# Optimization experiments

Measured on AMD Instinct MI355X. Metric: run time of the kernel, lower is better.

The kernel has to match this reference:

```python
import jax, jax.numpy as jnp
import numpy as np


def gcn_conv(x, edge_index, W, b):
    """PyG-style GCNConv: add self-loops, symmetric deg normalization,
    linear transform, scatter-add aggregation at destination nodes."""
    N = x.shape[0]
    loops = jnp.arange(N)
    src = jnp.concatenate([edge_index[0], loops])  # [E+N]
    dst = jnp.concatenate([edge_index[1], loops])  # [E+N]
    deg = jax.ops.segment_sum(jnp.ones_like(dst, dtype=x.dtype), dst, num_segments=N)
    dinv = jnp.where(deg > 0, deg ** -0.5, jnp.zeros_like(deg))
    norm = dinv[src] * dinv[dst]  # [E+N]
    h = x @ W  # [N, H] transform before propagate (as in PyG GCNConv)
    out = jax.ops.segment_sum(h[src] * norm[:, None], dst, num_segments=N)
    return out + b


def setup_inputs() -> dict:
    key = jax.random.key(0)
    ks = jax.random.split(key, 9)
    N, E, F_in, H, F_out = 100000, 3200000, 128, 16, 128
    x = jax.random.normal(ks[0], (N, F_in), dtype=jnp.float32)
    edge_index = jax.random.randint(ks[1], (2, E), 0, N, dtype=jnp.int64)
    s = lambda k, shp, fan_in: jax.random.normal(k, shp, dtype=jnp.float32) / np.sqrt(fan_in)
    return {
        "x": x,
        "edge_index": edge_index,
        "W1": s(ks[2], (F_in, H), F_in),
        "b1": jnp.zeros((H,), jnp.float32),
        "W2": s(ks[3], (H, H), H),
        "b2": jnp.zeros((H,), jnp.float32),
        "W_lin": s(ks[4], (H, F_out), H),
        "b_lin": jnp.zeros((F_out,), jnp.float32),
    }


def reference(x, edge_index, W1, b1, W2, b2, W_lin, b_lin):
    h = jax.nn.relu(gcn_conv(x, edge_index, W1, b1))
    h = jax.nn.relu(gcn_conv(h, edge_index, W2, b2))
    return h @ W_lin + b_lin
```

## Files before the change

kernel.cpp:

```cpp
#include <hip/hip_runtime.h>
#include <hip/hip_fp16.h>


typedef int   v4i __attribute__((ext_vector_type(4)));
typedef float v4f __attribute__((ext_vector_type(4)));
typedef float v2f __attribute__((ext_vector_type(2)));

#define NPB        256
#define NPB_SHIFT  8
#define NB_MAX     512
#define BCAP       10240
#define PART_TILE  8192
#define PART_THR   1024
#define PT_ITERS   (PART_TILE / 4 / PART_THR)
#define FXSCALE    262144.0f
#define FXINV      (1.0f / 262144.0f)

__global__ __launch_bounds__(NB_MAX) void k_initcur(int* __restrict__ cur) {
    cur[threadIdx.x] = threadIdx.x * BCAP;
}

__global__ __launch_bounds__(PART_THR) void k_partition(const int* __restrict__ ei,
                                                        int* __restrict__ cur,
                                                        int* __restrict__ pairs, int E) {
    __shared__ int h[NB_MAX];
    __shared__ int rb[NB_MAX];
    int t = threadIdx.x;
    const v4i* s4 = (const v4i*)ei;
    const v4i* d4 = (const v4i*)(ei + E);
    int EQ = E >> 2;
    int q0 = blockIdx.x * (PART_TILE / 4);
    bool last = (blockIdx.x == gridDim.x - 1);
    v4i dsave[PT_ITERS];

    for (int j = t; j < NB_MAX; j += PART_THR) h[j] = 0;
    __syncthreads();
#pragma unroll
    for (int it = 0; it < PT_ITERS; ++it) {
        int q = q0 + it * PART_THR + t;
        v4i dd;
        if (q < EQ) {
            dd = __builtin_nontemporal_load(d4 + q);
            atomicAdd(&h[dd.x >> NPB_SHIFT], 1);
            atomicAdd(&h[dd.y >> NPB_SHIFT], 1);
            atomicAdd(&h[dd.z >> NPB_SHIFT], 1);
            atomicAdd(&h[dd.w >> NPB_SHIFT], 1);
        }
        dsave[it] = dd;
    }
    if (last) {
        for (int e = (EQ << 2) + t; e < E; e += PART_THR)
            atomicAdd(&h[ei[E + e] >> NPB_SHIFT], 1);
    }
    __syncthreads();
    for (int j = t; j < NB_MAX; j += PART_THR) {
        int c = h[j];
        rb[j] = c ? atomicAdd(&cur[j], c) : 0;
        h[j] = 0;
    }
    __syncthreads();
#pragma unroll
    for (int it = 0; it < PT_ITERS; ++it) {
        int q = q0 + it * PART_THR + t;
        if (q < EQ) {
            v4i ss = __builtin_nontemporal_load(s4 + q);
            v4i dd = dsave[it];
#pragma unroll
            for (int k = 0; k < 4; ++k) {
                int s = ss[k], d = dd[k];
                int b = d >> NPB_SHIFT;
                int pos = rb[b] + atomicAdd(&h[b], 1);
                pairs[pos] = (s << NPB_SHIFT) | (d & (NPB - 1));
            }
        }
    }
    if (last) {
        for (int e = (EQ << 2) + t; e < E; e += PART_THR) {
            int s = ei[e], d = ei[E + e];
            int b = d >> NPB_SHIFT;
            int pos = rb[b] + atomicAdd(&h[b], 1);
            pairs[pos] = (s << NPB_SHIFT) | (d & (NPB - 1));
        }
    }
}

__global__ __launch_bounds__(256) void k_deg(const int* __restrict__ pairs,
                                             const int* __restrict__ cur,
                                             float* __restrict__ dinv, int N) {
    __shared__ int deg[NPB];
    int b = blockIdx.x, t = threadIdx.x;
    int base = b * BCAP;
    int cnt  = cur[b] - base;
    deg[t] = 0;
    __syncthreads();
    const v4i* p4 = (const v4i*)(pairs + base);
    int cq = cnt >> 2;
    for (int q = t; q < cq; q += 256) {
        v4i pp = __builtin_nontemporal_load(p4 + q);
        atomicAdd(&deg[pp.x & (NPB - 1)], 1);
        atomicAdd(&deg[pp.y & (NPB - 1)], 1);
        atomicAdd(&deg[pp.z & (NPB - 1)], 1);
        atomicAdd(&deg[pp.w & (NPB - 1)], 1);
    }
    for (int i = (cq << 2) + t; i < cnt; i += 256)
        atomicAdd(&deg[pairs[base + i] & (NPB - 1)], 1);
    __syncthreads();
    int n = (b << NPB_SHIFT) + t;
    if (n < N) dinv[n] = rsqrtf((float)(deg[t] + 1));
}

__global__ __launch_bounds__(256) void k_xform1(const float* __restrict__ x,
                                                const float* __restrict__ W1,
                                                const float* __restrict__ dinv,
                                                __half* __restrict__ g, int N) {
    __shared__ float xs[16][132];
    __shared__ float ws[128 * 16];
    int t = threadIdx.x;
    int n0 = blockIdx.x * 16;
    const v4f* w4 = (const v4f*)W1;
    const v4f* x4 = (const v4f*)x;
    for (int idx = t; idx < 512; idx += 256) ((v4f*)ws)[idx] = w4[idx];
    for (int idx = t; idx < 512; idx += 256) {
        int r = idx >> 5, c4 = idx & 31;
        int n = n0 + r;
        v4f v = (n < N) ? x4[(size_t)n * 32 + c4] : (v4f)(0.f);
        *(v4f*)&xs[r][c4 * 4] = v;
    }
    __syncthreads();
    int node = t >> 4, f = t & 15;
    int n = n0 + node;
    if (n < N) {
        float sum = 0.f;
#pragma unroll
        for (int k = 0; k < 128; ++k) sum += xs[node][k] * ws[k * 16 + f];
        g[(size_t)n * 16 + f] = __float2half_rn(sum * dinv[n]);
    }
}

__device__ __forceinline__ v4i gather16(const __half* __restrict__ g, int p, int fo) {
    return *(const v4i*)(g + (size_t)(p >> NPB_SHIFT) * 16 + fo);
}
__device__ __forceinline__ void commit8(int* __restrict__ acc, int p, int fo, v4i r) {
    int* a = &acc[(p & (NPB - 1)) * 17 + fo];
#pragma unroll
    for (int j = 0; j < 4; ++j) {
        float2 f = __half22float2(((const __half2*)&r)[j]);
        atomicAdd(a + 2 * j,     __float2int_rn(f.x * FXSCALE));
        atomicAdd(a + 2 * j + 1, __float2int_rn(f.y * FXSCALE));
    }
}

__global__ __launch_bounds__(1024) void k_aggr1e(const __half* __restrict__ g1,
                                                 const int* __restrict__ pairs,
                                                 const int* __restrict__ cur,
                                                 const float* __restrict__ dinv,
                                                 const float* __restrict__ b1,
                                                 const float* __restrict__ W2,
                                                 __half* __restrict__ g2, int N) {
    __shared__ int   acc[NPB * 17];
    __shared__ float w2s[256];
    __shared__ float b1s[16];
    int t = threadIdx.x, b = blockIdx.x;
    int n0 = b << NPB_SHIFT;
    int base = b * BCAP;
    int cnt  = cur[b] - base;
    const int* pb = pairs + base;
    if (t < 256) w2s[t] = W2[t];
    if (t < 16)  b1s[t] = b1[t];
    for (int i = t; i < NPB * 17; i += 1024) acc[i] = 0;
    __syncthreads();
    int es = t >> 1, fo = (t & 1) << 3;
    int e = es;
    for (; e + 1536 < cnt; e += 2048) {
        int p0 = __builtin_nontemporal_load(pb + e);
        int p1 = __builtin_nontemporal_load(pb + e + 512);
        int p2 = __builtin_nontemporal_load(pb + e + 1024);
        int p3 = __builtin_nontemporal_load(pb + e + 1536);
        v4i r0 = gather16(g1, p0, fo);
        v4i r1 = gather16(g1, p1, fo);
        v4i r2 = gather16(g1, p2, fo);
        v4i r3 = gather16(g1, p3, fo);
        commit8(acc, p0, fo, r0);
        commit8(acc, p1, fo, r1);
        commit8(acc, p2, fo, r2);
        commit8(acc, p3, fo, r3);
    }
    for (; e < cnt; e += 512) {
        int p0 = pb[e];
        commit8(acc, p0, fo, gather16(g1, p0, fo));
    }
    __syncthreads();
#pragma unroll
    for (int r = 0; r < 4; ++r) {
        int idx = r * 1024 + t;
        int d = idx >> 4, f = idx & 15;
        int n = n0 + d;
        float hv = 0.f;
        if (n < N) {
            float sum  = (float)acc[d * 17 + f] * FXINV;
            float self = __half2float(g1[(size_t)n * 16 + f]);
            hv = fmaxf(dinv[n] * (sum + self) + b1s[f], 0.f);
        }
        acc[d * 17 + f] = __float_as_int(hv);
    }
    __syncthreads();
#pragma unroll
    for (int r = 0; r < 2; ++r) {
        int idx2 = r * 1024 + t;
        int d = idx2 >> 3, ff = idx2 & 7;
        int n = n0 + d;
        if (n < N) {
            float sx = 0.f, sy = 0.f;
#pragma unroll
            for (int k = 0; k < 16; ++k) {
                float hv = __int_as_float(acc[d * 17 + k]);
                sx += hv * w2s[k * 16 + 2 * ff];
                sy += hv * w2s[k * 16 + 2 * ff + 1];
            }
            float di = dinv[n];
            *(__half2*)(g2 + (size_t)n * 16 + 2 * ff) = __floats2half2_rn(sx * di, sy * di);
        }
    }
}

__global__ __launch_bounds__(1024) void k_aggr2e(const __half* __restrict__ g2,
                                                 const int* __restrict__ pairs,
                                                 const int* __restrict__ cur,
                                                 const float* __restrict__ dinv,
                                                 const float* __restrict__ b2,
                                                 const float* __restrict__ Wl,
                                                 const float* __restrict__ bl,
                                                 float* __restrict__ out, int N) {
    __shared__ int   acc[NPB * 17];
    __shared__ float wls[16 * 128];
    __shared__ float bls[128];
    __shared__ float b2s[16];
    int t = threadIdx.x, b = blockIdx.x;
    int n0 = b << NPB_SHIFT;
    int base = b * BCAP;
    int cnt  = cur[b] - base;
    const int* pb = pairs + base;
    if (t < 512) ((v4f*)wls)[t] = ((const v4f*)Wl)[t];
    if (t < 128) bls[t] = bl[t];
    if (t < 16)  b2s[t] = b2[t];
    for (int i = t; i < NPB * 17; i += 1024) acc[i] = 0;
    __syncthreads();
    int es = t >> 1, fo = (t & 1) << 3;
    int e = es;
    for (; e + 1536 < cnt; e += 2048) {
        int p0 = __builtin_nontemporal_load(pb + e);
        int p1 = __builtin_nontemporal_load(pb + e + 512);
        int p2 = __builtin_nontemporal_load(pb + e + 1024);
        int p3 = __builtin_nontemporal_load(pb + e + 1536);
        v4i r0 = gather16(g2, p0, fo);
        v4i r1 = gather16(g2, p1, fo);
        v4i r2 = gather16(g2, p2, fo);
        v4i r3 = gather16(g2, p3, fo);
        commit8(acc, p0, fo, r0);
        commit8(acc, p1, fo, r1);
        commit8(acc, p2, fo, r2);
        commit8(acc, p3, fo, r3);
    }
    for (; e < cnt; e += 512) {
        int p0 = pb[e];
        commit8(acc, p0, fo, gather16(g2, p0, fo));
    }
    __syncthreads();
#pragma unroll
    for (int r = 0; r < 4; ++r) {
        int idx = r * 1024 + t;
        int d = idx >> 4, f = idx & 15;
        int n = n0 + d;
        float hv = 0.f;
        if (n < N) {
            float sum  = (float)acc[d * 17 + f] * FXINV;
            float self = __half2float(g2[(size_t)n * 16 + f]);
            hv = fmaxf(dinv[n] * (sum + self) + b2s[f], 0.f);
        }
        acc[d * 17 + f] = __float_as_int(hv);
    }
    __syncthreads();
    const v2f* wl2 = (const v2f*)wls;
#pragma unroll
    for (int r = 0; r < 16; ++r) {
        int idx2 = r * 1024 + t;
        int d = idx2 >> 6, fc = idx2 & 63;
        int n = n0 + d;
        if (n < N) {
            float ox = bls[2 * fc], oy = bls[2 * fc + 1];
#pragma unroll
            for (int k = 0; k < 16; ++k) {
                float hv = __int_as_float(acc[d * 17 + k]);
                v2f w = wl2[k * 64 + fc];
                ox += hv * w.x;
                oy += hv * w.y;
            }
            v2f o; o.x = ox; o.y = oy;
            __builtin_nontemporal_store(o, (v2f*)(out + (size_t)n * 128 + 2 * fc));
        }
    }
}

extern "C" void kernel_launch(void* const* d_in, const int* in_sizes, int n_in,
                              void* d_out, int out_size, void* d_ws, size_t ws_size,
                              hipStream_t stream) {
    const float* x  = (const float*)d_in[0];
    const int*   ei = (const int*)d_in[1];
    const float* W1 = (const float*)d_in[2];
    const float* b1 = (const float*)d_in[3];
    const float* W2 = (const float*)d_in[4];
    const float* b2 = (const float*)d_in[5];
    const float* Wl = (const float*)d_in[6];
    const float* bl = (const float*)d_in[7];
    float*       out = (float*)d_out;

    const int N = in_sizes[0] / 128;
    const int E = in_sizes[1] / 2;
    const int NB = (N + NPB - 1) >> NPB_SHIFT;

    char* ws = (char*)d_ws;
    auto carve = [&](size_t bytes) {
        char* p = ws;
        ws += (bytes + 255) & ~(size_t)255;
        return p;
    };
    int*    cur   = (int*)carve((size_t)NB_MAX * 4);
    float*  dinv  = (float*)carve((size_t)N * 4);
    int*    pairs = (int*)carve((size_t)NB_MAX * BCAP * 4);
    __half* g1    = (__half*)carve((size_t)N * 16 * 2);
    __half* g2    = (__half*)carve((size_t)N * 16 * 2);
    (void)ws_size; (void)n_in; (void)out_size;

    k_initcur<<<1, NB_MAX, 0, stream>>>(cur);
    k_partition<<<(E + PART_TILE - 1) / PART_TILE, PART_THR, 0, stream>>>(ei, cur, pairs, E);
    k_deg<<<NB, 256, 0, stream>>>(pairs, cur, dinv, N);
    k_xform1<<<(N + 15) / 16, 256, 0, stream>>>(x, W1, dinv, g1, N);
    k_aggr1e<<<NB, 1024, 0, stream>>>(g1, pairs, cur, dinv, b1, W2, g2, N);
    k_aggr2e<<<NB, 1024, 0, stream>>>(g2, pairs, cur, dinv, b2, Wl, bl, out, N);
}
```

Before: 253.5 us.

## Halve destination bucket size and fold degree counting into partition kernel

Shrinks each destination bucket from 256 to 128 nodes, which doubles the bucket count (about 782 blocks instead of 391) and halves the aggregation block size to 512 threads, so more of the GPU is busy during the gather and scatter phases. It also drops the separate k_deg pass. In-degrees are now counted with global atomics inside k_partition, and dinv is computed in k_xform1. The cost is 3.2M global atomics on random addresses plus a memset, in place of one extra read of the pairs array. The smaller bucket capacity leaves less slack against overflow.

```diff
diff --git a/kernel.cpp b/kernel.cpp
--- a/kernel.cpp
+++ b/kernel.cpp
@@ -6,10 +6,10 @@
 typedef float v4f __attribute__((ext_vector_type(4)));
 typedef float v2f __attribute__((ext_vector_type(2)));
 
-#define NPB        256
-#define NPB_SHIFT  8
-#define NB_MAX     512
-#define BCAP       10240
+#define NPB        128
+#define NPB_SHIFT  7
+#define NB_MAX     1024
+#define BCAP       5632
 #define PART_TILE  8192
 #define PART_THR   1024
 #define PT_ITERS   (PART_TILE / 4 / PART_THR)
@@ -22,7 +22,8 @@
 
 __global__ __launch_bounds__(PART_THR) void k_partition(const int* __restrict__ ei,
                                                         int* __restrict__ cur,
-                                                        int* __restrict__ pairs, int E) {
+                                                        int* __restrict__ pairs,
+                                                        int* __restrict__ deg, int E) {
     __shared__ int h[NB_MAX];
     __shared__ int rb[NB_MAX];
     int t = threadIdx.x;
@@ -45,12 +46,19 @@
             atomicAdd(&h[dd.y >> NPB_SHIFT], 1);
             atomicAdd(&h[dd.z >> NPB_SHIFT], 1);
             atomicAdd(&h[dd.w >> NPB_SHIFT], 1);
+            atomicAdd(&deg[dd.x], 1);
+            atomicAdd(&deg[dd.y], 1);
+            atomicAdd(&deg[dd.z], 1);
+            atomicAdd(&deg[dd.w], 1);
         }
         dsave[it] = dd;
     }
     if (last) {
-        for (int e = (EQ << 2) + t; e < E; e += PART_THR)
-            atomicAdd(&h[ei[E + e] >> NPB_SHIFT], 1);
+        for (int e = (EQ << 2) + t; e < E; e += PART_THR) {
+            int d = ei[E + e];
+            atomicAdd(&h[d >> NPB_SHIFT], 1);
+            atomicAdd(&deg[d], 1);
+        }
     }
     __syncthreads();
     for (int j = t; j < NB_MAX; j += PART_THR) {
@@ -84,37 +92,14 @@
     }
 }
 
-__global__ __launch_bounds__(256) void k_deg(const int* __restrict__ pairs,
-                                             const int* __restrict__ cur,
-                                             float* __restrict__ dinv, int N) {
-    __shared__ int deg[NPB];
-    int b = blockIdx.x, t = threadIdx.x;
-    int base = b * BCAP;
-    int cnt  = cur[b] - base;
-    deg[t] = 0;
-    __syncthreads();
-    const v4i* p4 = (const v4i*)(pairs + base);
-    int cq = cnt >> 2;
-    for (int q = t; q < cq; q += 256) {
-        v4i pp = __builtin_nontemporal_load(p4 + q);
-        atomicAdd(&deg[pp.x & (NPB - 1)], 1);
-        atomicAdd(&deg[pp.y & (NPB - 1)], 1);
-        atomicAdd(&deg[pp.z & (NPB - 1)], 1);
-        atomicAdd(&deg[pp.w & (NPB - 1)], 1);
-    }
-    for (int i = (cq << 2) + t; i < cnt; i += 256)
-        atomicAdd(&deg[pairs[base + i] & (NPB - 1)], 1);
-    __syncthreads();
-    int n = (b << NPB_SHIFT) + t;
-    if (n < N) dinv[n] = rsqrtf((float)(deg[t] + 1));
-}
-
 __global__ __launch_bounds__(256) void k_xform1(const float* __restrict__ x,
                                                 const float* __restrict__ W1,
-                                                const float* __restrict__ dinv,
+                                                const int* __restrict__ deg,
+                                                float* __restrict__ dinv,
                                                 __half* __restrict__ g, int N) {
     __shared__ float xs[16][132];
     __shared__ float ws[128 * 16];
+    __shared__ float dvs[16];
     int t = threadIdx.x;
     int n0 = blockIdx.x * 16;
     const v4f* w4 = (const v4f*)W1;
@@ -126,6 +111,14 @@
         v4f v = (n < N) ? x4[(size_t)n * 32 + c4] : (v4f)(0.f);
         *(v4f*)&xs[r][c4 * 4] = v;
     }
+    if (t < 16) {
+        int n = n0 + t;
+        if (n < N) {
+            float dv = rsqrtf((float)(deg[n] + 1));
+            dinv[n] = dv;
+            dvs[t] = dv;
+        }
+    }
     __syncthreads();
     int node = t >> 4, f = t & 15;
     int n = n0 + node;
@@ -133,7 +126,7 @@
         float sum = 0.f;
 #pragma unroll
         for (int k = 0; k < 128; ++k) sum += xs[node][k] * ws[k * 16 + f];
-        g[(size_t)n * 16 + f] = __float2half_rn(sum * dinv[n]);
+        g[(size_t)n * 16 + f] = __float2half_rn(sum * dvs[node]);
     }
 }
 
@@ -150,13 +143,13 @@
     }
 }
 
-__global__ __launch_bounds__(1024) void k_aggr1e(const __half* __restrict__ g1,
-                                                 const int* __restrict__ pairs,
-                                                 const int* __restrict__ cur,
-                                                 const float* __restrict__ dinv,
-                                                 const float* __restrict__ b1,
-                                                 const float* __restrict__ W2,
-                                                 __half* __restrict__ g2, int N) {
+__global__ __launch_bounds__(512) void k_aggr1e(const __half* __restrict__ g1,
+                                                const int* __restrict__ pairs,
+                                                const int* __restrict__ cur,
+                                                const float* __restrict__ dinv,
+                                                const float* __restrict__ b1,
+                                                const float* __restrict__ W2,
+                                                __half* __restrict__ g2, int N) {
     __shared__ int   acc[NPB * 17];
     __shared__ float w2s[256];
     __shared__ float b1s[16];
@@ -167,15 +160,15 @@
     const int* pb = pairs + base;
     if (t < 256) w2s[t] = W2[t];
     if (t < 16)  b1s[t] = b1[t];
-    for (int i = t; i < NPB * 17; i += 1024) acc[i] = 0;
+    for (int i = t; i < NPB * 17; i += 512) acc[i] = 0;
     __syncthreads();
     int es = t >> 1, fo = (t & 1) << 3;
     int e = es;
-    for (; e + 1536 < cnt; e += 2048) {
+    for (; e + 768 < cnt; e += 1024) {
         int p0 = __builtin_nontemporal_load(pb + e);
-        int p1 = __builtin_nontemporal_load(pb + e + 512);
-        int p2 = __builtin_nontemporal_load(pb + e + 1024);
-        int p3 = __builtin_nontemporal_load(pb + e + 1536);
+        int p1 = __builtin_nontemporal_load(pb + e + 256);
+        int p2 = __builtin_nontemporal_load(pb + e + 512);
+        int p3 = __builtin_nontemporal_load(pb + e + 768);
         v4i r0 = gather16(g1, p0, fo);
         v4i r1 = gather16(g1, p1, fo);
         v4i r2 = gather16(g1, p2, fo);
@@ -185,14 +178,14 @@
         commit8(acc, p2, fo, r2);
         commit8(acc, p3, fo, r3);
     }
-    for (; e < cnt; e += 512) {
+    for (; e < cnt; e += 256) {
         int p0 = pb[e];
         commit8(acc, p0, fo, gather16(g1, p0, fo));
     }
     __syncthreads();
 #pragma unroll
     for (int r = 0; r < 4; ++r) {
-        int idx = r * 1024 + t;
+        int idx = r * 512 + t;
         int d = idx >> 4, f = idx & 15;
         int n = n0 + d;
         float hv = 0.f;
@@ -206,7 +199,7 @@
     __syncthreads();
 #pragma unroll
     for (int r = 0; r < 2; ++r) {
-        int idx2 = r * 1024 + t;
+        int idx2 = r * 512 + t;
         int d = idx2 >> 3, ff = idx2 & 7;
         int n = n0 + d;
         if (n < N) {
@@ -223,14 +216,14 @@
     }
 }
 
-__global__ __launch_bounds__(1024) void k_aggr2e(const __half* __restrict__ g2,
-                                                 const int* __restrict__ pairs,
-                                                 const int* __restrict__ cur,
-                                                 const float* __restrict__ dinv,
-                                                 const float* __restrict__ b2,
-                                                 const float* __restrict__ Wl,
-                                                 const float* __restrict__ bl,
-                                                 float* __restrict__ out, int N) {
+__global__ __launch_bounds__(512) void k_aggr2e(const __half* __restrict__ g2,
+                                                const int* __restrict__ pairs,
+                                                const int* __restrict__ cur,
+                                                const float* __restrict__ dinv,
+                                                const float* __restrict__ b2,
+                                                const float* __restrict__ Wl,
+                                                const float* __restrict__ bl,
+                                                float* __restrict__ out, int N) {
     __shared__ int   acc[NPB * 17];
     __shared__ float wls[16 * 128];
     __shared__ float bls[128];
@@ -240,18 +233,18 @@
     int base = b * BCAP;
     int cnt  = cur[b] - base;
     const int* pb = pairs + base;
-    if (t < 512) ((v4f*)wls)[t] = ((const v4f*)Wl)[t];
+    ((v4f*)wls)[t] = ((const v4f*)Wl)[t];
     if (t < 128) bls[t] = bl[t];
     if (t < 16)  b2s[t] = b2[t];
-    for (int i = t; i < NPB * 17; i += 1024) acc[i] = 0;
+    for (int i = t; i < NPB * 17; i += 512) acc[i] = 0;
     __syncthreads();
     int es = t >> 1, fo = (t & 1) << 3;
     int e = es;
-    for (; e + 1536 < cnt; e += 2048) {
+    for (; e + 768 < cnt; e += 1024) {
         int p0 = __builtin_nontemporal_load(pb + e);
-        int p1 = __builtin_nontemporal_load(pb + e + 512);
-        int p2 = __builtin_nontemporal_load(pb + e + 1024);
-        int p3 = __builtin_nontemporal_load(pb + e + 1536);
+        int p1 = __builtin_nontemporal_load(pb + e + 256);
+        int p2 = __builtin_nontemporal_load(pb + e + 512);
+        int p3 = __builtin_nontemporal_load(pb + e + 768);
         v4i r0 = gather16(g2, p0, fo);
         v4i r1 = gather16(g2, p1, fo);
         v4i r2 = gather16(g2, p2, fo);
@@ -261,14 +254,14 @@
         commit8(acc, p2, fo, r2);
         commit8(acc, p3, fo, r3);
     }
-    for (; e < cnt; e += 512) {
+    for (; e < cnt; e += 256) {
         int p0 = pb[e];
         commit8(acc, p0, fo, gather16(g2, p0, fo));
     }
     __syncthreads();
 #pragma unroll
     for (int r = 0; r < 4; ++r) {
-        int idx = r * 1024 + t;
+        int idx = r * 512 + t;
         int d = idx >> 4, f = idx & 15;
         int n = n0 + d;
         float hv = 0.f;
@@ -283,7 +276,7 @@
     const v2f* wl2 = (const v2f*)wls;
 #pragma unroll
     for (int r = 0; r < 16; ++r) {
-        int idx2 = r * 1024 + t;
+        int idx2 = r * 512 + t;
         int d = idx2 >> 6, fc = idx2 & 63;
         int n = n0 + d;
         if (n < N) {
@@ -325,16 +318,17 @@
         return p;
     };
     int*    cur   = (int*)carve((size_t)NB_MAX * 4);
+    int*    deg   = (int*)carve((size_t)N * 4);
     float*  dinv  = (float*)carve((size_t)N * 4);
     int*    pairs = (int*)carve((size_t)NB_MAX * BCAP * 4);
     __half* g1    = (__half*)carve((size_t)N * 16 * 2);
     __half* g2    = (__half*)carve((size_t)N * 16 * 2);
     (void)ws_size; (void)n_in; (void)out_size;
 
+    hipMemsetAsync(deg, 0, (size_t)N * 4, stream);
     k_initcur<<<1, NB_MAX, 0, stream>>>(cur);
-    k_partition<<<(E + PART_TILE - 1) / PART_TILE, PART_THR, 0, stream>>>(ei, cur, pairs, E);
-    k_deg<<<NB, 256, 0, stream>>>(pairs, cur, dinv, N);
-    k_xform1<<<(N + 15) / 16, 256, 0, stream>>>(x, W1, dinv, g1, N);
-    k_aggr1e<<<NB, 1024, 0, stream>>>(g1, pairs, cur, dinv, b1, W2, g2, N);
-    k_aggr2e<<<NB, 1024, 0, stream>>>(g2, pairs, cur, dinv, b2, Wl, bl, out, N);
-}
+    k_partition<<<(E + PART_TILE - 1) / PART_TILE, PART_THR, 0, stream>>>(ei, cur, pairs, deg, E);
+    k_xform1<<<(N + 15) / 16, 256, 0, stream>>>(x, W1, deg, dinv, g1, N);
+    k_aggr1e<<<NB, 512, 0, stream>>>(g1, pairs, cur, dinv, b1, W2, g2, N);
+    k_aggr2e<<<NB, 512, 0, stream>>>(g2, pairs, cur, dinv, b2, Wl, bl, out, N);
+}
```

New measurement: 359.6 us. 41.9% more time.

## Use 196-node buckets via multiply-shift and fix partition grid to 512 blocks

Applied to the files above, without the earlier changes.

Bucket size drops from 256 to 196 nodes, computed with a magic-multiply division, so about 511 buckets are used instead of 391. The aggregation kernels then get more blocks and fill more CUs. The partition kernel now uses a fixed 512-block grid with a strided loop and reloads dst instead of keeping it in registers. The risks are extra integer multiplies, idle threads in the epilogue, and a smaller bucket capacity of 8192, which stays safe only while bucket occupancy keeps enough headroom.

```diff
diff --git a/kernel.cpp b/kernel.cpp
--- a/kernel.cpp
+++ b/kernel.cpp
@@ -6,80 +6,74 @@
 typedef float v4f __attribute__((ext_vector_type(4)));
 typedef float v2f __attribute__((ext_vector_type(2)));
 
-#define NPB        256
-#define NPB_SHIFT  8
+#define NPB        196
 #define NB_MAX     512
-#define BCAP       10240
-#define PART_TILE  8192
-#define PART_THR   1024
-#define PT_ITERS   (PART_TILE / 4 / PART_THR)
+#define BCAP       8192
+#define PACK_SHIFT 8
+#define PACK_MASK  255
+#define PART_GRID  512
 #define FXSCALE    262144.0f
 #define FXINV      (1.0f / 262144.0f)
 
+__device__ __forceinline__ int bucket_of(int d) {
+    return (int)(((unsigned long long)(unsigned)d * 87652394ull) >> 34);
+}
+
 __global__ __launch_bounds__(NB_MAX) void k_initcur(int* __restrict__ cur) {
     cur[threadIdx.x] = threadIdx.x * BCAP;
 }
 
-__global__ __launch_bounds__(PART_THR) void k_partition(const int* __restrict__ ei,
-                                                        int* __restrict__ cur,
-                                                        int* __restrict__ pairs, int E) {
+__global__ __launch_bounds__(1024) void k_partition(const int* __restrict__ ei,
+                                                    int* __restrict__ cur,
+                                                    int* __restrict__ pairs,
+                                                    int E, int QT) {
     __shared__ int h[NB_MAX];
     __shared__ int rb[NB_MAX];
     int t = threadIdx.x;
     const v4i* s4 = (const v4i*)ei;
     const v4i* d4 = (const v4i*)(ei + E);
     int EQ = E >> 2;
-    int q0 = blockIdx.x * (PART_TILE / 4);
+    int Q0 = blockIdx.x * QT;
+    int Q1 = min(Q0 + QT, EQ);
     bool last = (blockIdx.x == gridDim.x - 1);
-    v4i dsave[PT_ITERS];
-
-    for (int j = t; j < NB_MAX; j += PART_THR) h[j] = 0;
-    __syncthreads();
-#pragma unroll
-    for (int it = 0; it < PT_ITERS; ++it) {
-        int q = q0 + it * PART_THR + t;
-        v4i dd;
-        if (q < EQ) {
-            dd = __builtin_nontemporal_load(d4 + q);
-            atomicAdd(&h[dd.x >> NPB_SHIFT], 1);
-            atomicAdd(&h[dd.y >> NPB_SHIFT], 1);
-            atomicAdd(&h[dd.z >> NPB_SHIFT], 1);
-            atomicAdd(&h[dd.w >> NPB_SHIFT], 1);
-        }
-        dsave[it] = dd;
+
+    for (int j = t; j < NB_MAX; j += 1024) h[j] = 0;
+    __syncthreads();
+    for (int q = Q0 + t; q < Q1; q += 1024) {
+        v4i dd = __builtin_nontemporal_load(d4 + q);
+        atomicAdd(&h[bucket_of(dd.x)], 1);
+        atomicAdd(&h[bucket_of(dd.y)], 1);
+        atomicAdd(&h[bucket_of(dd.z)], 1);
+        atomicAdd(&h[bucket_of(dd.w)], 1);
     }
     if (last) {
-        for (int e = (EQ << 2) + t; e < E; e += PART_THR)
-            atomicAdd(&h[ei[E + e] >> NPB_SHIFT], 1);
-    }
-    __syncthreads();
-    for (int j = t; j < NB_MAX; j += PART_THR) {
+        for (int e = (EQ << 2) + t; e < E; e += 1024)
+            atomicAdd(&h[bucket_of(ei[E + e])], 1);
+    }
+    __syncthreads();
+    for (int j = t; j < NB_MAX; j += 1024) {
         int c = h[j];
         rb[j] = c ? atomicAdd(&cur[j], c) : 0;
         h[j] = 0;
     }
     __syncthreads();
-#pragma unroll
-    for (int it = 0; it < PT_ITERS; ++it) {
-        int q = q0 + it * PART_THR + t;
-        if (q < EQ) {
-            v4i ss = __builtin_nontemporal_load(s4 + q);
-            v4i dd = dsave[it];
-#pragma unroll
-            for (int k = 0; k < 4; ++k) {
-                int s = ss[k], d = dd[k];
-                int b = d >> NPB_SHIFT;
-                int pos = rb[b] + atomicAdd(&h[b], 1);
-                pairs[pos] = (s << NPB_SHIFT) | (d & (NPB - 1));
-            }
+    for (int q = Q0 + t; q < Q1; q += 1024) {
+        v4i ss = __builtin_nontemporal_load(s4 + q);
+        v4i dd = __builtin_nontemporal_load(d4 + q);
+#pragma unroll
+        for (int k = 0; k < 4; ++k) {
+            int s = ss[k], d = dd[k];
+            int b = bucket_of(d);
+            int pos = rb[b] + atomicAdd(&h[b], 1);
+            pairs[pos] = (s << PACK_SHIFT) | (d - b * NPB);
         }
     }
     if (last) {
-        for (int e = (EQ << 2) + t; e < E; e += PART_THR) {
+        for (int e = (EQ << 2) + t; e < E; e += 1024) {
             int s = ei[e], d = ei[E + e];
-            int b = d >> NPB_SHIFT;
+            int b = bucket_of(d);
             int pos = rb[b] + atomicAdd(&h[b], 1);
-            pairs[pos] = (s << NPB_SHIFT) | (d & (NPB - 1));
+            pairs[pos] = (s << PACK_SHIFT) | (d - b * NPB);
         }
     }
 }
@@ -91,22 +85,22 @@
     int b = blockIdx.x, t = threadIdx.x;
     int base = b * BCAP;
     int cnt  = cur[b] - base;
-    deg[t] = 0;
+    if (t < NPB) deg[t] = 0;
     __syncthreads();
     const v4i* p4 = (const v4i*)(pairs + base);
     int cq = cnt >> 2;
     for (int q = t; q < cq; q += 256) {
         v4i pp = __builtin_nontemporal_load(p4 + q);
-        atomicAdd(&deg[pp.x & (NPB - 1)], 1);
-        atomicAdd(&deg[pp.y & (NPB - 1)], 1);
-        atomicAdd(&deg[pp.z & (NPB - 1)], 1);
-        atomicAdd(&deg[pp.w & (NPB - 1)], 1);
+        atomicAdd(&deg[pp.x & PACK_MASK], 1);
+        atomicAdd(&deg[pp.y & PACK_MASK], 1);
+        atomicAdd(&deg[pp.z & PACK_MASK], 1);
+        atomicAdd(&deg[pp.w & PACK_MASK], 1);
     }
     for (int i = (cq << 2) + t; i < cnt; i += 256)
-        atomicAdd(&deg[pairs[base + i] & (NPB - 1)], 1);
-    __syncthreads();
-    int n = (b << NPB_SHIFT) + t;
-    if (n < N) dinv[n] = rsqrtf((float)(deg[t] + 1));
+        atomicAdd(&deg[pairs[base + i] & PACK_MASK], 1);
+    __syncthreads();
+    int n = b * NPB + t;
+    if (t < NPB && n < N) dinv[n] = rsqrtf((float)(deg[t] + 1));
 }
 
 __global__ __launch_bounds__(256) void k_xform1(const float* __restrict__ x,
@@ -138,10 +132,10 @@
 }
 
 __device__ __forceinline__ v4i gather16(const __half* __restrict__ g, int p, int fo) {
-    return *(const v4i*)(g + (size_t)(p >> NPB_SHIFT) * 16 + fo);
+    return *(const v4i*)(g + (size_t)(p >> PACK_SHIFT) * 16 + fo);
 }
 __device__ __forceinline__ void commit8(int* __restrict__ acc, int p, int fo, v4i r) {
-    int* a = &acc[(p & (NPB - 1)) * 17 + fo];
+    int* a = &acc[(p & PACK_MASK) * 17 + fo];
 #pragma unroll
     for (int j = 0; j < 4; ++j) {
         float2 f = __half22float2(((const __half2*)&r)[j]);
@@ -161,7 +155,7 @@
     __shared__ float w2s[256];
     __shared__ float b1s[16];
     int t = threadIdx.x, b = blockIdx.x;
-    int n0 = b << NPB_SHIFT;
+    int n0 = b * NPB;
     int base = b * BCAP;
     int cnt  = cur[b] - base;
     const int* pb = pairs + base;
@@ -193,32 +187,36 @@
 #pragma unroll
     for (int r = 0; r < 4; ++r) {
         int idx = r * 1024 + t;
-        int d = idx >> 4, f = idx & 15;
-        int n = n0 + d;
-        float hv = 0.f;
-        if (n < N) {
-            float sum  = (float)acc[d * 17 + f] * FXINV;
-            float self = __half2float(g1[(size_t)n * 16 + f]);
-            hv = fmaxf(dinv[n] * (sum + self) + b1s[f], 0.f);
-        }
-        acc[d * 17 + f] = __float_as_int(hv);
+        if (idx < NPB * 16) {
+            int d = idx >> 4, f = idx & 15;
+            int n = n0 + d;
+            float hv = 0.f;
+            if (n < N) {
+                float sum  = (float)acc[d * 17 + f] * FXINV;
+                float self = __half2float(g1[(size_t)n * 16 + f]);
+                hv = fmaxf(dinv[n] * (sum + self) + b1s[f], 0.f);
+            }
+            acc[d * 17 + f] = __float_as_int(hv);
+        }
     }
     __syncthreads();
 #pragma unroll
     for (int r = 0; r < 2; ++r) {
         int idx2 = r * 1024 + t;
-        int d = idx2 >> 3, ff = idx2 & 7;
-        int n = n0 + d;
-        if (n < N) {
-            float sx = 0.f, sy = 0.f;
-#pragma unroll
-            for (int k = 0; k < 16; ++k) {
-                float hv = __int_as_float(acc[d * 17 + k]);
-                sx += hv * w2s[k * 16 + 2 * ff];
-                sy += hv * w2s[k * 16 + 2 * ff + 1];
+        if (idx2 < NPB * 8) {
+            int d = idx2 >> 3, ff = idx2 & 7;
+            int n = n0 + d;
+            if (n < N) {
+                float sx = 0.f, sy = 0.f;
+#pragma unroll
+                for (int k = 0; k < 16; ++k) {
+                    float hv = __int_as_float(acc[d * 17 + k]);
+                    sx += hv * w2s[k * 16 + 2 * ff];
+                    sy += hv * w2s[k * 16 + 2 * ff + 1];
+                }
+                float di = dinv[n];
+                *(__half2*)(g2 + (size_t)n * 16 + 2 * ff) = __floats2half2_rn(sx * di, sy * di);
             }
-            float di = dinv[n];
-            *(__half2*)(g2 + (size_t)n * 16 + 2 * ff) = __floats2half2_rn(sx * di, sy * di);
         }
     }
 }
@@ -236,7 +234,7 @@
     __shared__ float bls[128];
     __shared__ float b2s[16];
     int t = threadIdx.x, b = blockIdx.x;
-    int n0 = b << NPB_SHIFT;
+    int n0 = b * NPB;
     int base = b * BCAP;
     int cnt  = cur[b] - base;
     const int* pb = pairs + base;
@@ -269,34 +267,38 @@
 #pragma unroll
     for (int r = 0; r < 4; ++r) {
         int idx = r * 1024 + t;
-        int d = idx >> 4, f = idx & 15;
-        int n = n0 + d;
-        float hv = 0.f;
-        if (n < N) {
-            float sum  = (float)acc[d * 17 + f] * FXINV;
-            float self = __half2float(g2[(size_t)n * 16 + f]);
-            hv = fmaxf(dinv[n] * (sum + self) + b2s[f], 0.f);
-        }
-        acc[d * 17 + f] = __float_as_int(hv);
+        if (idx < NPB * 16) {
+            int d = idx >> 4, f = idx & 15;
+            int n = n0 + d;
+            float hv = 0.f;
+            if (n < N) {
+                float sum  = (float)acc[d * 17 + f] * FXINV;
+                float self = __half2float(g2[(size_t)n * 16 + f]);
+                hv = fmaxf(dinv[n] * (sum + self) + b2s[f], 0.f);
+            }
+            acc[d * 17 + f] = __float_as_int(hv);
+        }
     }
     __syncthreads();
     const v2f* wl2 = (const v2f*)wls;
 #pragma unroll
-    for (int r = 0; r < 16; ++r) {
+    for (int r = 0; r < 13; ++r) {
         int idx2 = r * 1024 + t;
-        int d = idx2 >> 6, fc = idx2 & 63;
-        int n = n0 + d;
-        if (n < N) {
-            float ox = bls[2 * fc], oy = bls[2 * fc + 1];
-#pragma unroll
-            for (int k = 0; k < 16; ++k) {
-                float hv = __int_as_float(acc[d * 17 + k]);
-                v2f w = wl2[k * 64 + fc];
-                ox += hv * w.x;
-                oy += hv * w.y;
+        if (idx2 < NPB * 64) {
+            int d = idx2 >> 6, fc = idx2 & 63;
+            int n = n0 + d;
+            if (n < N) {
+                float ox = bls[2 * fc], oy = bls[2 * fc + 1];
+#pragma unroll
+                for (int k = 0; k < 16; ++k) {
+                    float hv = __int_as_float(acc[d * 17 + k]);
+                    v2f w = wl2[k * 64 + fc];
+                    ox += hv * w.x;
+                    oy += hv * w.y;
+                }
+                v2f o; o.x = ox; o.y = oy;
+                __builtin_nontemporal_store(o, (v2f*)(out + (size_t)n * 128 + 2 * fc));
             }
-            v2f o; o.x = ox; o.y = oy;
-            __builtin_nontemporal_store(o, (v2f*)(out + (size_t)n * 128 + 2 * fc));
         }
     }
 }
@@ -316,7 +318,9 @@
 
     const int N = in_sizes[0] / 128;
     const int E = in_sizes[1] / 2;
-    const int NB = (N + NPB - 1) >> NPB_SHIFT;
+    const int NB = (N + NPB - 1) / NPB;
+    const int EQ = E >> 2;
+    const int QT = (EQ + PART_GRID - 1) / PART_GRID;
 
     char* ws = (char*)d_ws;
     auto carve = [&](size_t bytes) {
@@ -332,7 +336,7 @@
     (void)ws_size; (void)n_in; (void)out_size;
 
     k_initcur<<<1, NB_MAX, 0, stream>>>(cur);
-    k_partition<<<(E + PART_TILE - 1) / PART_TILE, PART_THR, 0, stream>>>(ei, cur, pairs, E);
+    k_partition<<<PART_GRID, 1024, 0, stream>>>(ei, cur, pairs, E, QT);
     k_deg<<<NB, 256, 0, stream>>>(pairs, cur, dinv, N);
     k_xform1<<<(N + 15) / 16, 256, 0, stream>>>(x, W1, dinv, g1, N);
     k_aggr1e<<<NB, 1024, 0, stream>>>(g1, pairs, cur, dinv, b1, W2, g2, N);
```

Measured after the change: 237.9 us. 6.2% less time.
